# Optimization experiments

Measured on AMD Instinct MI355X. Metric: run time of the kernel, lower is better.

## Reference

```python
import jax, jax.numpy as jnp
import numpy as np

B, S, D, H = 4, 2048, 1024, 16
HD = D // H  # 64


def setup_inputs() -> dict:
    key = jax.random.key(0)
    ks = jax.random.split(key, 12)
    s = 1.0 / np.sqrt(D)
    return {
        "q": jax.random.normal(ks[0], (B, S, D), jnp.float32),
        "k": jax.random.normal(ks[1], (B, S, D), jnp.float32),
        "v": jax.random.normal(ks[2], (B, S, D), jnp.float32),
        "mask": jnp.zeros((B, 1, 1, S), jnp.float32),
        "Wq": jax.random.normal(ks[3], (D, D), jnp.float32) * s,
        "bq": jnp.zeros((D,), jnp.float32),
        "Wk": jax.random.normal(ks[4], (D, D), jnp.float32) * s,
        "bk": jnp.zeros((D,), jnp.float32),
        "Wv": jax.random.normal(ks[5], (D, D), jnp.float32) * s,
        "bv": jnp.zeros((D,), jnp.float32),
        "Wo": jax.random.normal(ks[6], (D, D), jnp.float32) * s,
        "bo": jnp.zeros((D,), jnp.float32),
    }


def _split_heads(x):
    # [B, S, D] -> [B, H, S, HD]
    b, s, _ = x.shape
    return x.reshape(b, s, H, HD).transpose(0, 2, 1, 3)


def reference(q, k, v, mask, Wq, bq, Wk, bk, Wv, bv, Wo, bo):
    _q = _split_heads(q @ Wq + bq)
    _k = _split_heads(k @ Wk + bk)
    _v = _split_heads(v @ Wv + bv)
    # NOTE: original scales by (head_dim + 1e-8), NOT sqrt(head_dim)
    score = jnp.einsum("bhqd,bhkd->bhqk", _q, _k) / (HD + 1e-8)
    score = score + mask * (-1e9)
    attn = jax.nn.softmax(score, axis=-1)
    out = jnp.einsum("bhqk,bhkd->bhqd", attn, _v)  # [B, H, S, HD]
    out = out.transpose(0, 2, 1, 3).reshape(q.shape[0], q.shape[1], D)
    # dropout in inference mode -> identity
    return out @ Wo + bo
```

## Files before the change

### kernel.cpp

```cpp
#include <hip/hip_runtime.h>

#define DN 1024
#define SN 2048
#define BATCH 4
#define HN 16
#define HDN 64

typedef __attribute__((ext_vector_type(8))) short bf16x8;
typedef __attribute__((ext_vector_type(4))) float f32x4;
typedef __attribute__((ext_vector_type(16))) float f32x16;
typedef __attribute__((ext_vector_type(4))) unsigned int u32x4;

static __device__ __forceinline__ unsigned short f2b(float f) {
  unsigned u = __float_as_uint(f);
  unsigned r = (u + 0x7fffu + ((u >> 16) & 1u)) >> 16;
  return (unsigned short)r;
}

static __device__ __forceinline__ void gload16(const void* g, const void* l) {
  __builtin_amdgcn_global_load_lds(
      (const __attribute__((address_space(1))) unsigned int*)g,
      (__attribute__((address_space(3))) unsigned int*)l, 16, 0, 0);
}

static __device__ __forceinline__ float vmax16(const f32x16& v) {
  float a0 = fmaxf(v[0], v[1]), a1 = fmaxf(v[2], v[3]);
  float a2 = fmaxf(v[4], v[5]), a3 = fmaxf(v[6], v[7]);
  float a4 = fmaxf(v[8], v[9]), a5 = fmaxf(v[10], v[11]);
  float a6 = fmaxf(v[12], v[13]), a7 = fmaxf(v[14], v[15]);
  float b0 = fmaxf(a0, a1), b1 = fmaxf(a2, a3);
  float b2 = fmaxf(a4, a5), b3 = fmaxf(a6, a7);
  return fmaxf(fmaxf(b0, b1), fmaxf(b2, b3));
}

static __device__ __forceinline__ float vsum16(const f32x16& v) {
  float a0 = v[0] + v[1], a1 = v[2] + v[3];
  float a2 = v[4] + v[5], a3 = v[6] + v[7];
  float a4 = v[8] + v[9], a5 = v[10] + v[11];
  float a6 = v[12] + v[13], a7 = v[14] + v[15];
  float b0 = a0 + a1, b1 = a2 + a3, b2 = a4 + a5, b3 = a6 + a7;
  return (b0 + b1) + (b2 + b3);
}

static __device__ __forceinline__ unsigned cvtpk(float lo, float hi) {
  unsigned w;
  asm volatile("v_cvt_pk_bf16_f32 %0, %1, %2" : "=v"(w) : "v"(lo), "v"(hi));
  return w;
}

__global__ void wtrans(const float* __restrict__ W0, const float* __restrict__ W1,
                       const float* __restrict__ W2, const float* __restrict__ W3,
                       unsigned short* __restrict__ Wt) {
  __shared__ float tile[32][33];
  const int z = blockIdx.z;
  const float* W = (z == 0) ? W0 : (z == 1) ? W1 : (z == 2) ? W2 : W3;
  const int tx = threadIdx.x, ty = threadIdx.y;
  const int n0 = blockIdx.x * 32, k0 = blockIdx.y * 32;
#pragma unroll
  for (int j = ty; j < 32; j += 8)
    tile[j][tx] = W[(long)(k0 + j) * DN + n0 + tx];
  __syncthreads();
  unsigned short* o = Wt + (long)z * DN * DN;
#pragma unroll
  for (int j = ty; j < 32; j += 8)
    o[(long)(n0 + j) * DN + k0 + tx] = f2b(tile[tx][j]);
}

__global__ void cvtbf16(const float* __restrict__ x, unsigned short* __restrict__ y) {
  const float4* xv = (const float4*)x;
  ushort4* yv = (ushort4*)y;
  for (int i = blockIdx.x * 256 + threadIdx.x; i < (8192 * 1024 / 4); i += 2048 * 256) {
    float4 vv = xv[i];
    ushort4 o;
    o.x = f2b(vv.x); o.y = f2b(vv.y); o.z = f2b(vv.z); o.w = f2b(vv.w);
    yv[i] = o;
  }
}

template <int OUTMODE>
__global__ __launch_bounds__(256, 2) void gemm128(
    const unsigned short* __restrict__ A, const unsigned short* __restrict__ Bt,
    const float* __restrict__ bias, void* __restrict__ Cout, int M, int N, int K) {
  __shared__ unsigned short Asm[128 * 32];
  __shared__ unsigned short Bsm[128 * 32];
  const int t = threadIdx.x;
  const int lane = t & 63, w = t >> 6;
  const int rl = lane & 15, g = lane >> 4;
  const int wm = (w >> 1) << 6, wn = (w & 1) << 6;
  const long bm = (long)blockIdx.x * 128, bn = (long)blockIdx.y * 128;

  f32x4 acc[4][4] = {};

  const int c0 = t, c1 = 256 + t;
  const int r0 = c0 >> 2, s0 = c0 & 3;
  const int r1 = c1 >> 2, s1 = c1 & 3;

  for (int k0 = 0; k0 < K; k0 += 32) {
    __syncthreads();
    gload16(A + (bm + r0) * K + k0 + s0 * 8, Asm + (w << 6) * 8);
    gload16(A + (bm + r1) * K + k0 + s1 * 8, Asm + (256 + (w << 6)) * 8);
    gload16(Bt + (bn + r0) * K + k0 + s0 * 8, Bsm + (w << 6) * 8);
    gload16(Bt + (bn + r1) * K + k0 + s1 * 8, Bsm + (256 + (w << 6)) * 8);
    asm volatile("s_waitcnt vmcnt(0)" ::: "memory");
    __syncthreads();
    bf16x8 af[4], bfr[4];
#pragma unroll
    for (int mf = 0; mf < 4; ++mf)
      af[mf] = *(const bf16x8*)(Asm + (wm + mf * 16 + rl) * 32 + g * 8);
#pragma unroll
    for (int nf = 0; nf < 4; ++nf)
      bfr[nf] = *(const bf16x8*)(Bsm + (wn + nf * 16 + rl) * 32 + g * 8);
#pragma unroll
    for (int mf = 0; mf < 4; ++mf)
#pragma unroll
      for (int nf = 0; nf < 4; ++nf)
        acc[mf][nf] = __builtin_amdgcn_mfma_f32_16x16x32_bf16(af[mf], bfr[nf], acc[mf][nf], 0, 0, 0);
  }

#pragma unroll
  for (int mf = 0; mf < 4; ++mf)
#pragma unroll
    for (int nf = 0; nf < 4; ++nf) {
      long col = bn + wn + nf * 16 + rl;
      float bv = bias[col];
      if (OUTMODE == 2) {
        long row0 = bm + wm + mf * 16 + g * 4;
        long bb = row0 >> 11, ss = row0 & 2047;
        ushort4 pack;
        pack.x = f2b(acc[mf][nf][0] + bv);
        pack.y = f2b(acc[mf][nf][1] + bv);
        pack.z = f2b(acc[mf][nf][2] + bv);
        pack.w = f2b(acc[mf][nf][3] + bv);
        *(ushort4*)((unsigned short*)Cout + (bb * DN + col) * SN + ss) = pack;
      } else {
#pragma unroll
        for (int r = 0; r < 4; ++r) {
          long row = bm + wm + mf * 16 + g * 4 + r;
          float vv = acc[mf][nf][r] + bv;
          if (OUTMODE == 1)
            ((float*)Cout)[row * N + col] = vv;
          else
            ((unsigned short*)Cout)[row * N + col] = f2b(vv);
        }
      }
    }
}

__global__ __launch_bounds__(256, 4) void attnk(
    const unsigned short* __restrict__ Qh, const unsigned short* __restrict__ Kh,
    const unsigned short* __restrict__ Vt, const float* __restrict__ mask,
    unsigned short* __restrict__ AO) {
  const int t = threadIdx.x, lane = t & 63, w = t >> 6;
  const int ql = lane & 31, hi = lane >> 5;
  const int qb = blockIdx.x * 128;
  const int h = blockIdx.y, b = blockIdx.z;

  __shared__ unsigned short KV[2][8192];
  __shared__ float ms[SN];

  const unsigned short* Kp = Kh + (long)b * SN * DN + h * HDN;
  const unsigned short* Vp = Vt + ((long)b * DN + h * HDN) * SN;

  {
    const float4* mp = (const float4*)(mask + (long)b * SN);
    float4* md = (float4*)ms;
    float4 v0 = mp[t], v1 = mp[256 + t];
    v0.x *= -1e9f; v0.y *= -1e9f; v0.z *= -1e9f; v0.w *= -1e9f;
    v1.x *= -1e9f; v1.y *= -1e9f; v1.z *= -1e9f; v1.w *= -1e9f;
    md[t] = v0;
    md[256 + t] = v1;
  }

  const unsigned short* Qp = Qh + ((long)b * SN + qb + (w << 5) + ql) * DN + h * HDN;
  bf16x8 qf[4];
#pragma unroll
  for (int f = 0; f < 4; ++f)
    qf[f] = *(const bf16x8*)(Qp + f * 16 + hi * 8);

#define STAGE(buf, tt)                                                          \
  {                                                                             \
    const int base_ = (tt) * 64;                                                \
    _Pragma("unroll") for (int i_ = 0; i_ < 2; ++i_) {                          \
      int c_ = i_ * 256 + t;                                                    \
      int r_ = c_ >> 3, sl_ = c_ & 7;                                           \
      gload16(Kp + (long)(base_ + r_) * DN + ((sl_ ^ (r_ & 7)) << 3),           \
              &KV[buf][(i_ * 256 + (w << 6)) * 8]);                             \
      gload16(Vp + (long)r_ * SN + base_ + ((sl_ ^ (r_ & 7)) << 3),             \
              &KV[buf][4096 + (i_ * 256 + (w << 6)) * 8]);                      \
    }                                                                           \
  }

  STAGE(0, 0);
  asm volatile("s_waitcnt vmcnt(0)" ::: "memory");
  __syncthreads();

  f32x16 O[2] = {};
  float m_run = -1e30f, l_run = 0.f;
  const float ISC = 0.015625f;

  for (int tt = 0; tt < SN / 64; ++tt) {
    const int cur = tt & 1;
    if (tt < SN / 64 - 1) STAGE(cur ^ 1, tt + 1);
    const unsigned short* Kb = &KV[cur][0];
    const unsigned short* Vb = &KV[cur][4096];

    f32x16 s[2] = {};
#pragma unroll
    for (int f = 0; f < 4; ++f) {
      const int kr0 = ql, kr1 = 32 + ql;
      bf16x8 a0 = *(const bf16x8*)(Kb + kr0 * 64 + (((f * 2 + hi) ^ (kr0 & 7)) << 3));
      bf16x8 a1 = *(const bf16x8*)(Kb + kr1 * 64 + (((f * 2 + hi) ^ (kr1 & 7)) << 3));
      s[0] = __builtin_amdgcn_mfma_f32_32x32x16_bf16(a0, qf[f], s[0], 0, 0, 0);
      s[1] = __builtin_amdgcn_mfma_f32_32x32x16_bf16(a1, qf[f], s[1], 0, 0, 0);
    }

#pragma unroll
    for (int j = 0; j < 4; ++j) {
      f32x4 m0 = *(const f32x4*)(ms + tt * 64 + 8 * j + 4 * hi);
      f32x4 m1 = *(const f32x4*)(ms + tt * 64 + 32 + 8 * j + 4 * hi);
#pragma unroll
      for (int i2 = 0; i2 < 4; ++i2) {
        s[0][4 * j + i2] = fmaf(s[0][4 * j + i2], ISC, m0[i2]);
        s[1][4 * j + i2] = fmaf(s[1][4 * j + i2], ISC, m1[i2]);
      }
    }

    float pm = fmaxf(vmax16(s[0]), vmax16(s[1]));
    pm = fmaxf(pm, __shfl_xor(pm, 32));
    if (__any(pm - m_run > 8.f)) {
      float mn = fmaxf(m_run, pm);
      float co = __expf(m_run - mn);
      m_run = mn;
      l_run *= co;
#pragma unroll
      for (int r = 0; r < 16; ++r) { O[0][r] *= co; O[1][r] *= co; }
    }
#pragma unroll
    for (int r = 0; r < 16; ++r) {
      s[0][r] = __expf(s[0][r] - m_run);
      s[1][r] = __expf(s[1][r] - m_run);
    }
    float rs = vsum16(s[0]) + vsum16(s[1]);
    rs += __shfl_xor(rs, 32);
    l_run += rs;

    unsigned aw[8], bw[8];
#pragma unroll
    for (int j = 0; j < 4; ++j) {
      aw[j]     = cvtpk(s[0][4 * j], s[0][4 * j + 1]);
      bw[j]     = cvtpk(s[0][4 * j + 2], s[0][4 * j + 3]);
      aw[4 + j] = cvtpk(s[1][4 * j], s[1][4 * j + 1]);
      bw[4 + j] = cvtpk(s[1][4 * j + 2], s[1][4 * j + 3]);
    }
    bf16x8 pb[4];
#pragma unroll
    for (int ks = 0; ks < 4; ++ks) {
      unsigned x0 = aw[2 * ks], y0 = aw[2 * ks + 1];
      unsigned x1 = bw[2 * ks], y1 = bw[2 * ks + 1];
      asm volatile("v_permlane32_swap_b32 %0, %1" : "+v"(x0), "+v"(y0));
      asm volatile("v_permlane32_swap_b32 %0, %1" : "+v"(x1), "+v"(y1));
      u32x4 wv = {x0, x1, y0, y1};
      pb[ks] = __builtin_bit_cast(bf16x8, wv);
    }

#pragma unroll
    for (int da = 0; da < 2; ++da) {
      const int dr = da * 32 + ql;
#pragma unroll
      for (int ks = 0; ks < 4; ++ks) {
        bf16x8 va = *(const bf16x8*)(Vb + dr * 64 + (((ks * 2 + hi) ^ (dr & 7)) << 3));
        O[da] = __builtin_amdgcn_mfma_f32_32x32x16_bf16(va, pb[ks], O[da], 0, 0, 0);
      }
    }

    asm volatile("s_waitcnt vmcnt(0)" ::: "memory");
    __syncthreads();
  }
#undef STAGE

  float inv = 1.0f / l_run;
  unsigned short* dst = AO + ((long)b * SN + qb + (w << 5) + ql) * DN + h * HDN;
#pragma unroll
  for (int da = 0; da < 2; ++da)
#pragma unroll
    for (int j = 0; j < 4; ++j) {
      ushort4 pk;
      pk.x = f2b(O[da][4 * j + 0] * inv);
      pk.y = f2b(O[da][4 * j + 1] * inv);
      pk.z = f2b(O[da][4 * j + 2] * inv);
      pk.w = f2b(O[da][4 * j + 3] * inv);
      *(ushort4*)(dst + da * 32 + 8 * j + 4 * hi) = pk;
    }
}

extern "C" void kernel_launch(void* const* d_in, const int* in_sizes, int n_in,
                              void* d_out, int out_size, void* d_ws, size_t ws_size,
                              hipStream_t stream) {
  (void)in_sizes; (void)n_in; (void)out_size; (void)ws_size;
  const float* q    = (const float*)d_in[0];
  const float* k    = (const float*)d_in[1];
  const float* v    = (const float*)d_in[2];
  const float* mask = (const float*)d_in[3];
  const float* Wq   = (const float*)d_in[4];
  const float* bq   = (const float*)d_in[5];
  const float* Wk   = (const float*)d_in[6];
  const float* bk   = (const float*)d_in[7];
  const float* Wv   = (const float*)d_in[8];
  const float* bv   = (const float*)d_in[9];
  const float* Wo   = (const float*)d_in[10];
  const float* bo   = (const float*)d_in[11];

  char* ws = (char*)d_ws;
  unsigned short* Xb = (unsigned short*)ws;
  unsigned short* Wt = (unsigned short*)(ws + (size_t)16777216);
  unsigned short* Qh = (unsigned short*)(ws + (size_t)16777216 + 8388608);
  unsigned short* Kh = Qh + (size_t)8192 * 1024;
  unsigned short* Vh = Kh + (size_t)8192 * 1024;

  wtrans<<<dim3(32, 32, 4), dim3(32, 8), 0, stream>>>(Wq, Wk, Wv, Wo, Wt);

  cvtbf16<<<2048, 256, 0, stream>>>(q, Xb);
  gemm128<0><<<dim3(64, 8), 256, 0, stream>>>(Xb, Wt + (size_t)0 * 1024 * 1024, bq,
                                              Qh, 8192, 1024, 1024);
  cvtbf16<<<2048, 256, 0, stream>>>(k, Xb);
  gemm128<0><<<dim3(64, 8), 256, 0, stream>>>(Xb, Wt + (size_t)1 * 1024 * 1024, bk,
                                              Kh, 8192, 1024, 1024);
  cvtbf16<<<2048, 256, 0, stream>>>(v, Xb);
  gemm128<2><<<dim3(64, 8), 256, 0, stream>>>(Xb, Wt + (size_t)2 * 1024 * 1024, bv,
                                              Vh, 8192, 1024, 1024);

  attnk<<<dim3(16, 16, 4), 256, 0, stream>>>(Qh, Kh, Vh, mask, Xb);

  gemm128<1><<<dim3(64, 8), 256, 0, stream>>>(Xb, Wt + (size_t)3 * 1024 * 1024, bo,
                                              d_out, 8192, 1024, 1024);
}
```

Measured before the change: 383.6 us.

## Fuse input conversion into batched QKV GEMM and streamline attention softmax

Drops the three separate fp32-to-bf16 conversion kernels. A single batched QKV GEMM launch now loads fp32 activations into LDS with an XOR swizzle and converts them to bf16 while building the MFMA fragments. The softmax scale and log2(e) are folded into Q at projection time, so attention can use exp2. The attention kernel also gets a fixed-threshold running max that starts at zero, a per-tile flag that skips mask loads when a mask tile is all zero, s_setprio around the MFMA blocks, and a Q load issued after the first K/V stage. This removes an intermediate activation round trip and kernel launches, and cuts softmax ALU work. In exchange, the GEMM stages twice as many A bytes through LDS, and the lazy-max scheme may lose precision when scores are strongly negative.

Measured after the change: 605.5 us. 57.8% more time.

```diff
diff --git a/kernel.cpp b/kernel.cpp
--- a/kernel.cpp
+++ b/kernel.cpp
@@ -11,6 +11,9 @@
 typedef __attribute__((ext_vector_type(16))) float f32x16;
 typedef __attribute__((ext_vector_type(4))) unsigned int u32x4;
 
+#define QSC 0.022542110013890054f
+#define MSC -1.4426950408889634e9f
+
 static __device__ __forceinline__ unsigned short f2b(float f) {
   unsigned u = __float_as_uint(f);
   unsigned r = (u + 0x7fffu + ((u >> 16) & 1u)) >> 16;
@@ -23,14 +26,21 @@
       (__attribute__((address_space(3))) unsigned int*)l, 16, 0, 0);
 }
 
+static __device__ __forceinline__ unsigned cvtpk(float lo, float hi) {
+  unsigned w;
+  asm volatile("v_cvt_pk_bf16_f32 %0, %1, %2" : "=v"(w) : "v"(lo), "v"(hi));
+  return w;
+}
+
 static __device__ __forceinline__ float vmax16(const f32x16& v) {
-  float a0 = fmaxf(v[0], v[1]), a1 = fmaxf(v[2], v[3]);
-  float a2 = fmaxf(v[4], v[5]), a3 = fmaxf(v[6], v[7]);
-  float a4 = fmaxf(v[8], v[9]), a5 = fmaxf(v[10], v[11]);
-  float a6 = fmaxf(v[12], v[13]), a7 = fmaxf(v[14], v[15]);
-  float b0 = fmaxf(a0, a1), b1 = fmaxf(a2, a3);
-  float b2 = fmaxf(a4, a5), b3 = fmaxf(a6, a7);
-  return fmaxf(fmaxf(b0, b1), fmaxf(b2, b3));
+  float t0 = fmaxf(fmaxf(v[0], v[1]), v[2]);
+  float t1 = fmaxf(fmaxf(v[3], v[4]), v[5]);
+  float t2 = fmaxf(fmaxf(v[6], v[7]), v[8]);
+  float t3 = fmaxf(fmaxf(v[9], v[10]), v[11]);
+  float t4 = fmaxf(fmaxf(v[12], v[13]), v[14]);
+  float u0 = fmaxf(fmaxf(t0, t1), t2);
+  float u1 = fmaxf(fmaxf(t3, t4), v[15]);
+  return fmaxf(u0, u1);
 }
 
 static __device__ __forceinline__ float vsum16(const f32x16& v) {
@@ -40,12 +50,6 @@
   float a6 = v[12] + v[13], a7 = v[14] + v[15];
   float b0 = a0 + a1, b1 = a2 + a3, b2 = a4 + a5, b3 = a6 + a7;
   return (b0 + b1) + (b2 + b3);
-}
-
-static __device__ __forceinline__ unsigned cvtpk(float lo, float hi) {
-  unsigned w;
-  asm volatile("v_cvt_pk_bf16_f32 %0, %1, %2" : "=v"(w) : "v"(lo), "v"(hi));
-  return w;
 }
 
 __global__ void wtrans(const float* __restrict__ W0, const float* __restrict__ W1,
@@ -66,39 +70,114 @@
     o[(long)(n0 + j) * DN + k0 + tx] = f2b(tile[tx][j]);
 }
 
-__global__ void cvtbf16(const float* __restrict__ x, unsigned short* __restrict__ y) {
-  const float4* xv = (const float4*)x;
-  ushort4* yv = (ushort4*)y;
-  for (int i = blockIdx.x * 256 + threadIdx.x; i < (8192 * 1024 / 4); i += 2048 * 256) {
-    float4 vv = xv[i];
-    ushort4 o;
-    o.x = f2b(vv.x); o.y = f2b(vv.y); o.z = f2b(vv.z); o.w = f2b(vv.w);
-    yv[i] = o;
-  }
-}
-
-template <int OUTMODE>
-__global__ __launch_bounds__(256, 2) void gemm128(
+__global__ __launch_bounds__(256, 2) void gemm_qkv(
+    const float* __restrict__ q, const float* __restrict__ k, const float* __restrict__ v,
+    const unsigned short* __restrict__ Wt,
+    const float* __restrict__ bq, const float* __restrict__ bk, const float* __restrict__ bv,
+    unsigned short* __restrict__ Qh, unsigned short* __restrict__ Kh,
+    unsigned short* __restrict__ Vh) {
+  const int z = blockIdx.z;
+  const float* A = (z == 0) ? q : (z == 1) ? k : v;
+  const unsigned short* Bt = Wt + (size_t)z * DN * DN;
+  const float* bias = (z == 0) ? bq : (z == 1) ? bk : bv;
+
+  __shared__ float As[128 * 32];
+  __shared__ unsigned short Bs[128 * 32];
+  const int t = threadIdx.x;
+  const int lane = t & 63, w = t >> 6;
+  const int rl = lane & 15, g = lane >> 4;
+  const int wm = (w >> 1) << 6, wn = (w & 1) << 6;
+  const long bm = (long)blockIdx.x * 128, bn = (long)blockIdx.y * 128;
+  const int K = DN;
+
+  f32x4 acc[4][4] = {};
+
+  for (int k0 = 0; k0 < K; k0 += 32) {
+    __syncthreads();
+#pragma unroll
+    for (int i = 0; i < 4; ++i) {
+      int c = i * 256 + t;
+      int r_ = c >> 3, sl = c & 7;
+      gload16(A + (bm + r_) * K + k0 + ((sl ^ (r_ & 7)) << 2), As + (i * 256 + (w << 6)) * 4);
+    }
+#pragma unroll
+    for (int i = 0; i < 2; ++i) {
+      int c = i * 256 + t;
+      int r_ = c >> 2, sl = c & 3;
+      gload16(Bt + (bn + r_) * K + k0 + sl * 8, Bs + (i * 256 + (w << 6)) * 8);
+    }
+    asm volatile("s_waitcnt vmcnt(0)" ::: "memory");
+    __syncthreads();
+
+    bf16x8 af[4], bfr[4];
+#pragma unroll
+    for (int mf = 0; mf < 4; ++mf) {
+      int r_ = wm + mf * 16 + rl;
+      const float* Ar = As + r_ * 32;
+      f32x4 lo = *(const f32x4*)(Ar + (((2 * g) ^ (r_ & 7)) << 2));
+      f32x4 hi = *(const f32x4*)(Ar + (((2 * g + 1) ^ (r_ & 7)) << 2));
+      u32x4 uw = {cvtpk(lo[0], lo[1]), cvtpk(lo[2], lo[3]),
+                  cvtpk(hi[0], hi[1]), cvtpk(hi[2], hi[3])};
+      af[mf] = __builtin_bit_cast(bf16x8, uw);
+    }
+#pragma unroll
+    for (int nf = 0; nf < 4; ++nf)
+      bfr[nf] = *(const bf16x8*)(Bs + (wn + nf * 16 + rl) * 32 + g * 8);
+#pragma unroll
+    for (int mf = 0; mf < 4; ++mf)
+#pragma unroll
+      for (int nf = 0; nf < 4; ++nf)
+        acc[mf][nf] = __builtin_amdgcn_mfma_f32_16x16x32_bf16(af[mf], bfr[nf], acc[mf][nf], 0, 0, 0);
+  }
+
+  const float scale = (z == 0) ? QSC : 1.0f;
+#pragma unroll
+  for (int mf = 0; mf < 4; ++mf)
+#pragma unroll
+    for (int nf = 0; nf < 4; ++nf) {
+      long col = bn + wn + nf * 16 + rl;
+      float bv2 = bias[col];
+      if (z == 2) {
+        long row0 = bm + wm + mf * 16 + g * 4;
+        long bb = row0 >> 11, ss = row0 & 2047;
+        ushort4 pack;
+        pack.x = f2b(acc[mf][nf][0] + bv2);
+        pack.y = f2b(acc[mf][nf][1] + bv2);
+        pack.z = f2b(acc[mf][nf][2] + bv2);
+        pack.w = f2b(acc[mf][nf][3] + bv2);
+        *(ushort4*)(Vh + (bb * DN + col) * SN + ss) = pack;
+      } else {
+        unsigned short* Cout = (z == 0) ? Qh : Kh;
+#pragma unroll
+        for (int r = 0; r < 4; ++r) {
+          long row = bm + wm + mf * 16 + g * 4 + r;
+          Cout[row * DN + col] = f2b((acc[mf][nf][r] + bv2) * scale);
+        }
+      }
+    }
+}
+
+__global__ __launch_bounds__(256, 2) void gemm_out(
     const unsigned short* __restrict__ A, const unsigned short* __restrict__ Bt,
-    const float* __restrict__ bias, void* __restrict__ Cout, int M, int N, int K) {
-  __shared__ unsigned short Asm[128 * 32];
+    const float* __restrict__ bias, float* __restrict__ Cout) {
+  __shared__ unsigned short Asm2[128 * 32];
   __shared__ unsigned short Bsm[128 * 32];
   const int t = threadIdx.x;
   const int lane = t & 63, w = t >> 6;
   const int rl = lane & 15, g = lane >> 4;
   const int wm = (w >> 1) << 6, wn = (w & 1) << 6;
   const long bm = (long)blockIdx.x * 128, bn = (long)blockIdx.y * 128;
+  const int K = DN, N = DN;
 
   f32x4 acc[4][4] = {};
-
   const int c0 = t, c1 = 256 + t;
   const int r0 = c0 >> 2, s0 = c0 & 3;
   const int r1 = c1 >> 2, s1 = c1 & 3;
 
   for (int k0 = 0; k0 < K; k0 += 32) {
     __syncthreads();
-    gload16(A + (bm + r0) * K + k0 + s0 * 8, Asm + (w << 6) * 8);
-    gload16(A + (bm + r1) * K + k0 + s1 * 8, Asm + (256 + (w << 6)) * 8);
+    gload16(A + (bm + r0) * K + k0 + s0 * 8, Asm2 + (w << 6) * 8);
+    gload16(A + (bm + r1) * K + k0 + s1 * 8, Asm2 + (256 + (w << 6)) * 8);
     gload16(Bt + (bn + r0) * K + k0 + s0 * 8, Bsm + (w << 6) * 8);
     gload16(Bt + (bn + r1) * K + k0 + s1 * 8, Bsm + (256 + (w << 6)) * 8);
     asm volatile("s_waitcnt vmcnt(0)" ::: "memory");
@@ -106,7 +185,7 @@
     bf16x8 af[4], bfr[4];
 #pragma unroll
     for (int mf = 0; mf < 4; ++mf)
-      af[mf] = *(const bf16x8*)(Asm + (wm + mf * 16 + rl) * 32 + g * 8);
+      af[mf] = *(const bf16x8*)(Asm2 + (wm + mf * 16 + rl) * 32 + g * 8);
 #pragma unroll
     for (int nf = 0; nf < 4; ++nf)
       bfr[nf] = *(const bf16x8*)(Bsm + (wn + nf * 16 + rl) * 32 + g * 8);
@@ -122,26 +201,11 @@
 #pragma unroll
     for (int nf = 0; nf < 4; ++nf) {
       long col = bn + wn + nf * 16 + rl;
-      float bv = bias[col];
-      if (OUTMODE == 2) {
-        long row0 = bm + wm + mf * 16 + g * 4;
-        long bb = row0 >> 11, ss = row0 & 2047;
-        ushort4 pack;
-        pack.x = f2b(acc[mf][nf][0] + bv);
-        pack.y = f2b(acc[mf][nf][1] + bv);
-        pack.z = f2b(acc[mf][nf][2] + bv);
-        pack.w = f2b(acc[mf][nf][3] + bv);
-        *(ushort4*)((unsigned short*)Cout + (bb * DN + col) * SN + ss) = pack;
-      } else {
-#pragma unroll
-        for (int r = 0; r < 4; ++r) {
-          long row = bm + wm + mf * 16 + g * 4 + r;
-          float vv = acc[mf][nf][r] + bv;
-          if (OUTMODE == 1)
-            ((float*)Cout)[row * N + col] = vv;
-          else
-            ((unsigned short*)Cout)[row * N + col] = f2b(vv);
-        }
+      float bv2 = bias[col];
+#pragma unroll
+      for (int r = 0; r < 4; ++r) {
+        long row = bm + wm + mf * 16 + g * 4 + r;
+        Cout[row * N + col] = acc[mf][nf][r] + bv2;
       }
     }
 }
@@ -165,17 +229,11 @@
     const float4* mp = (const float4*)(mask + (long)b * SN);
     float4* md = (float4*)ms;
     float4 v0 = mp[t], v1 = mp[256 + t];
-    v0.x *= -1e9f; v0.y *= -1e9f; v0.z *= -1e9f; v0.w *= -1e9f;
-    v1.x *= -1e9f; v1.y *= -1e9f; v1.z *= -1e9f; v1.w *= -1e9f;
+    v0.x *= MSC; v0.y *= MSC; v0.z *= MSC; v0.w *= MSC;
+    v1.x *= MSC; v1.y *= MSC; v1.z *= MSC; v1.w *= MSC;
     md[t] = v0;
     md[256 + t] = v1;
   }
-
-  const unsigned short* Qp = Qh + ((long)b * SN + qb + (w << 5) + ql) * DN + h * HDN;
-  bf16x8 qf[4];
-#pragma unroll
-  for (int f = 0; f < 4; ++f)
-    qf[f] = *(const bf16x8*)(Qp + f * 16 + hi * 8);
 
 #define STAGE(buf, tt)                                                          \
   {                                                                             \
@@ -191,12 +249,32 @@
   }
 
   STAGE(0, 0);
+
+  const unsigned short* Qp = Qh + ((long)b * SN + qb + (w << 5) + ql) * DN + h * HDN;
+  bf16x8 qf[4];
+#pragma unroll
+  for (int f = 0; f < 4; ++f)
+    qf[f] = *(const bf16x8*)(Qp + f * 16 + hi * 8);
+
   asm volatile("s_waitcnt vmcnt(0)" ::: "memory");
   __syncthreads();
 
+  unsigned mflags;
+  {
+    int mt = lane & 31;
+    const f32x4* mrow = (const f32x4*)(ms + mt * 64);
+    bool nz = false;
+#pragma unroll
+    for (int i2 = 0; i2 < 16; ++i2) {
+      f32x4 mv2 = mrow[i2];
+      nz = nz || (mv2[0] != 0.f) || (mv2[1] != 0.f) || (mv2[2] != 0.f) || (mv2[3] != 0.f);
+    }
+    unsigned long long bal = __ballot(nz);
+    mflags = (unsigned)bal | (unsigned)(bal >> 32);
+  }
+
   f32x16 O[2] = {};
-  float m_run = -1e30f, l_run = 0.f;
-  const float ISC = 0.015625f;
+  float m_run = 0.f, l_run = 0.f;
 
   for (int tt = 0; tt < SN / 64; ++tt) {
     const int cur = tt & 1;
@@ -204,53 +282,59 @@
     const unsigned short* Kb = &KV[cur][0];
     const unsigned short* Vb = &KV[cur][4096];
 
-    f32x16 s[2] = {};
+    f32x16 s0, s1;
+    if ((mflags >> tt) & 1u) {
+#pragma unroll
+      for (int j = 0; j < 4; ++j) {
+        f32x4 m0 = *(const f32x4*)(ms + tt * 64 + 8 * j + 4 * hi);
+        f32x4 m1 = *(const f32x4*)(ms + tt * 64 + 32 + 8 * j + 4 * hi);
+#pragma unroll
+        for (int i2 = 0; i2 < 4; ++i2) {
+          s0[4 * j + i2] = m0[i2] - m_run;
+          s1[4 * j + i2] = m1[i2] - m_run;
+        }
+      }
+    } else {
+#pragma unroll
+      for (int r = 0; r < 16; ++r) { s0[r] = -m_run; s1[r] = -m_run; }
+    }
+
+    __builtin_amdgcn_s_setprio(1);
 #pragma unroll
     for (int f = 0; f < 4; ++f) {
-      const int kr0 = ql, kr1 = 32 + ql;
-      bf16x8 a0 = *(const bf16x8*)(Kb + kr0 * 64 + (((f * 2 + hi) ^ (kr0 & 7)) << 3));
-      bf16x8 a1 = *(const bf16x8*)(Kb + kr1 * 64 + (((f * 2 + hi) ^ (kr1 & 7)) << 3));
-      s[0] = __builtin_amdgcn_mfma_f32_32x32x16_bf16(a0, qf[f], s[0], 0, 0, 0);
-      s[1] = __builtin_amdgcn_mfma_f32_32x32x16_bf16(a1, qf[f], s[1], 0, 0, 0);
-    }
-
-#pragma unroll
-    for (int j = 0; j < 4; ++j) {
-      f32x4 m0 = *(const f32x4*)(ms + tt * 64 + 8 * j + 4 * hi);
-      f32x4 m1 = *(const f32x4*)(ms + tt * 64 + 32 + 8 * j + 4 * hi);
-#pragma unroll
-      for (int i2 = 0; i2 < 4; ++i2) {
-        s[0][4 * j + i2] = fmaf(s[0][4 * j + i2], ISC, m0[i2]);
-        s[1][4 * j + i2] = fmaf(s[1][4 * j + i2], ISC, m1[i2]);
-      }
-    }
-
-    float pm = fmaxf(vmax16(s[0]), vmax16(s[1]));
+      bf16x8 a0 = *(const bf16x8*)(Kb + ql * 64 + (((f * 2 + hi) ^ (ql & 7)) << 3));
+      bf16x8 a1 = *(const bf16x8*)(Kb + (32 + ql) * 64 + (((f * 2 + hi) ^ (ql & 7)) << 3));
+      s0 = __builtin_amdgcn_mfma_f32_32x32x16_bf16(a0, qf[f], s0, 0, 0, 0);
+      s1 = __builtin_amdgcn_mfma_f32_32x32x16_bf16(a1, qf[f], s1, 0, 0, 0);
+    }
+    __builtin_amdgcn_s_setprio(0);
+
+    float pm = fmaxf(vmax16(s0), vmax16(s1));
     pm = fmaxf(pm, __shfl_xor(pm, 32));
-    if (__any(pm - m_run > 8.f)) {
-      float mn = fmaxf(m_run, pm);
-      float co = __expf(m_run - mn);
-      m_run = mn;
+    if (__any(pm > 11.5f)) {
+      float dd = fmaxf(pm, 0.f);
+      m_run += dd;
+      float co = exp2f(-dd);
       l_run *= co;
 #pragma unroll
       for (int r = 0; r < 16; ++r) { O[0][r] *= co; O[1][r] *= co; }
-    }
-#pragma unroll
-    for (int r = 0; r < 16; ++r) {
-      s[0][r] = __expf(s[0][r] - m_run);
-      s[1][r] = __expf(s[1][r] - m_run);
-    }
-    float rs = vsum16(s[0]) + vsum16(s[1]);
+#pragma unroll
+      for (int r = 0; r < 16; ++r) { s0[r] = exp2f(s0[r] - dd); s1[r] = exp2f(s1[r] - dd); }
+    } else {
+#pragma unroll
+      for (int r = 0; r < 16; ++r) { s0[r] = exp2f(s0[r]); s1[r] = exp2f(s1[r]); }
+    }
+    float rs = vsum16(s0) + vsum16(s1);
     rs += __shfl_xor(rs, 32);
     l_run += rs;
 
     unsigned aw[8], bw[8];
 #pragma unroll
     for (int j = 0; j < 4; ++j) {
-      aw[j]     = cvtpk(s[0][4 * j], s[0][4 * j + 1]);
-      bw[j]     = cvtpk(s[0][4 * j + 2], s[0][4 * j + 3]);
-      aw[4 + j] = cvtpk(s[1][4 * j], s[1][4 * j + 1]);
-      bw[4 + j] = cvtpk(s[1][4 * j + 2], s[1][4 * j + 3]);
+      aw[j]     = cvtpk(s0[4 * j], s0[4 * j + 1]);
+      bw[j]     = cvtpk(s0[4 * j + 2], s0[4 * j + 3]);
+      aw[4 + j] = cvtpk(s1[4 * j], s1[4 * j + 1]);
+      bw[4 + j] = cvtpk(s1[4 * j + 2], s1[4 * j + 3]);
     }
     bf16x8 pb[4];
 #pragma unroll
@@ -263,6 +347,7 @@
       pb[ks] = __builtin_bit_cast(bf16x8, wv);
     }
 
+    __builtin_amdgcn_s_setprio(1);
 #pragma unroll
     for (int da = 0; da < 2; ++da) {
       const int dr = da * 32 + ql;
@@ -272,6 +357,7 @@
         O[da] = __builtin_amdgcn_mfma_f32_32x32x16_bf16(va, pb[ks], O[da], 0, 0, 0);
       }
     }
+    __builtin_amdgcn_s_setprio(0);
 
     asm volatile("s_waitcnt vmcnt(0)" ::: "memory");
     __syncthreads();
@@ -311,7 +397,7 @@
   const float* bo   = (const float*)d_in[11];
 
   char* ws = (char*)d_ws;
-  unsigned short* Xb = (unsigned short*)ws;
+  unsigned short* AO = (unsigned short*)ws;
   unsigned short* Wt = (unsigned short*)(ws + (size_t)16777216);
   unsigned short* Qh = (unsigned short*)(ws + (size_t)16777216 + 8388608);
   unsigned short* Kh = Qh + (size_t)8192 * 1024;
@@ -319,18 +405,10 @@
 
   wtrans<<<dim3(32, 32, 4), dim3(32, 8), 0, stream>>>(Wq, Wk, Wv, Wo, Wt);
 
-  cvtbf16<<<2048, 256, 0, stream>>>(q, Xb);
-  gemm128<0><<<dim3(64, 8), 256, 0, stream>>>(Xb, Wt + (size_t)0 * 1024 * 1024, bq,
-                                              Qh, 8192, 1024, 1024);
-  cvtbf16<<<2048, 256, 0, stream>>>(k, Xb);
-  gemm128<0><<<dim3(64, 8), 256, 0, stream>>>(Xb, Wt + (size_t)1 * 1024 * 1024, bk,
-                                              Kh, 8192, 1024, 1024);
-  cvtbf16<<<2048, 256, 0, stream>>>(v, Xb);
-  gemm128<2><<<dim3(64, 8), 256, 0, stream>>>(Xb, Wt + (size_t)2 * 1024 * 1024, bv,
-                                              Vh, 8192, 1024, 1024);
-
-  attnk<<<dim3(16, 16, 4), 256, 0, stream>>>(Qh, Kh, Vh, mask, Xb);
-
-  gemm128<1><<<dim3(64, 8), 256, 0, stream>>>(Xb, Wt + (size_t)3 * 1024 * 1024, bo,
-                                              d_out, 8192, 1024, 1024);
-}
+  gemm_qkv<<<dim3(64, 8, 3), 256, 0, stream>>>(q, k, v, Wt, bq, bk, bv, Qh, Kh, Vh);
+
+  attnk<<<dim3(16, 16, 4), 256, 0, stream>>>(Qh, Kh, Vh, mask, AO);
+
+  gemm_out<<<dim3(64, 8), 256, 0, stream>>>(AO, Wt + (size_t)3 * 1024 * 1024, bo,
+                                            (float*)d_out);
+}
```
